# Kernel tuning notes

Measured on AMD Instinct MI355X. Metric: run time of the kernel, lower is better.

## Reference

```python
import jax, jax.numpy as jnp
import numpy as np

NUM_RBF = 300
RADIUS_RES = 0.1
GAMMA = 10.0
HIDDEN = 64
MB, ATOM = 32, 64


def setup_inputs() -> dict:
    key = jax.random.key(0)
    ks = jax.random.split(key, 12)
    def lin(kw, kb, fan_in, fan_out):
        lim = 1.0 / np.sqrt(fan_in)
        W = jax.random.uniform(kw, (fan_out, fan_in), jnp.float32, -lim, lim)
        b = jax.random.uniform(kb, (fan_out,), jnp.float32, -lim, lim)
        return W, b
    W1, b1 = lin(ks[0], ks[1], HIDDEN, HIDDEN)
    W2, b2 = lin(ks[2], ks[3], HIDDEN, HIDDEN)
    W3, b3 = lin(ks[4], ks[5], HIDDEN, HIDDEN)
    Wd1, bd1 = lin(ks[6], ks[7], NUM_RBF, HIDDEN)
    Wd2, bd2 = lin(ks[8], ks[9], HIDDEN, HIDDEN)
    x = jax.random.normal(ks[10], (MB, ATOM, HIDDEN), jnp.float32)
    dist = jax.random.uniform(ks[11], (MB, ATOM, ATOM), jnp.float32, 0.0, 10.0)
    return {"x": x, "dist": dist,
            "W1": W1, "b1": b1, "W2": W2, "b2": b2, "W3": W3, "b3": b3,
            "Wd1": Wd1, "bd1": bd1, "Wd2": Wd2, "bd2": bd2}


def reference(x, dist, W1, b1, W2, b2, W3, b3, Wd1, bd1, Wd2, bd2):
    sp = jax.nn.softplus
    # linear1 applied per-atom
    v = jnp.einsum('mic,oc->mio', x, W1) + b1                      # [mb, atom, h]
    # CFConv: gaussian RBF expansion of pairwise distances
    centers = jnp.arange(NUM_RBF, dtype=jnp.float32) * RADIUS_RES  # [rbf]
    rbf = jnp.exp(-GAMMA * (dist[..., None] - centers) ** 2)       # [mb, a, a, rbf]
    # 2-layer filter MLP on each pair
    f = sp(jnp.einsum('mijr,hr->mijh', rbf, Wd1) + bd1)            # [mb, a, a, h]
    f = sp(jnp.einsum('mijh,oh->mijo', f, Wd2) + bd2)              # [mb, a, a, h]
    # broadcast-multiply v over pairs and reduce over source atom i (dim=1)
    v = jnp.einsum('mic,mijc->mjc', v, f)                          # [mb, atom, h]
    v = sp(jnp.einsum('mic,oc->mio', v, W2) + b2)
    v = jnp.einsum('mic,oc->mio', v, W3) + b3
    return x + v
```

## Files before the change

kernel.cpp:

```cpp
#include <hip/hip_runtime.h>
#include <math.h>

#define MB_    32
#define ATOM_  64
#define HID_   64
#define NRBF_  300
#define GAMMA_ 10.0f
#define RES_   0.1f

#define TPTS      2001
#define TSTEP     0.005f
#define INV_TSTEP 200.0f

#define RWIN 28

#define T_OFF   0
#define T_SZ    (TPTS * 64)
#define V1_OFF  (T_OFF + T_SZ)
#define V1_SZ   (MB_ * 64 * 64)
#define W2T_OFF (V1_OFF + V1_SZ)
#define W3T_OFF (W2T_OFF + 4096)

__device__ __forceinline__ float sp_f(float x) {
    return fmaxf(x, 0.f) + log1pf(__expf(-fabsf(x)));
}

__global__ __launch_bounds__(256)
void schnet_prep(const float* __restrict__ x,   const float* __restrict__ W1,
                 const float* __restrict__ b1,  const float* __restrict__ W2,
                 const float* __restrict__ W3,  const float* __restrict__ Wd1,
                 const float* __restrict__ bd1, const float* __restrict__ Wd2,
                 const float* __restrict__ bd2, float* __restrict__ ws)
{
    __shared__ float smem[8320];
    const int tid = threadIdx.x;
    const int b   = blockIdx.x;

    if (b < MB_) {
        float* sx = smem;
        float* sw = smem + 4160;
        const float* xm = x + b * 4096;
        for (int e = tid; e < 4096; e += 256) {
            int i = e >> 6, c = e & 63;
            sx[i * 65 + c] = xm[e];
            sw[i * 65 + c] = W1[e];
        }
        __syncthreads();
        const int tx = tid & 15;
        const int ty = tid >> 4;
        float acc[4][4];
        #pragma unroll
        for (int aa = 0; aa < 4; ++aa)
            #pragma unroll
            for (int bb = 0; bb < 4; ++bb)
                acc[aa][bb] = b1[4 * tx + bb];
        #pragma unroll 8
        for (int k = 0; k < 64; ++k) {
            float xa[4], wb[4];
            #pragma unroll
            for (int aa = 0; aa < 4; ++aa) xa[aa] = sx[(4 * ty + aa) * 65 + k];
            #pragma unroll
            for (int bb = 0; bb < 4; ++bb) wb[bb] = sw[(4 * tx + bb) * 65 + k];
            #pragma unroll
            for (int aa = 0; aa < 4; ++aa)
                #pragma unroll
                for (int bb = 0; bb < 4; ++bb)
                    acc[aa][bb] = fmaf(xa[aa], wb[bb], acc[aa][bb]);
        }
        #pragma unroll
        for (int aa = 0; aa < 4; ++aa) {
            float4 v = make_float4(acc[aa][0], acc[aa][1], acc[aa][2], acc[aa][3]);
            *(float4*)(ws + V1_OFF + (b * 64 + 4 * ty + aa) * 64 + 4 * tx) = v;
        }
    } else if (b < MB_ + 501) {
        float* su = smem;
        const int sub = tid >> 6, c = tid & 63;
        const int s  = (b - MB_) * 4 + sub;
        const int se = min(s, TPTS - 1);
        const float d = se * TSTEP;

        int r0 = (int)ceilf((d - 1.35f) * 10.0f);
        r0 = max(r0, 0);

        float a0 = bd1[c], a1 = 0.f;
        const float* wrow1 = Wd1 + c * NRBF_ + r0;
        #pragma unroll
        for (int k = 0; k < RWIN; k += 2) {
            float t0 = fmaf(-RES_, (float)(r0 + k),     d);
            float t1 = fmaf(-RES_, (float)(r0 + k + 1), d);
            float w0 = __expf(-GAMMA_ * t0 * t0);
            float w1 = __expf(-GAMMA_ * t1 * t1);
            a0 = fmaf(w0, wrow1[k],     a0);
            a1 = fmaf(w1, wrow1[k + 1], a1);
        }
        su[sub * 64 + c] = sp_f(a0 + a1);
        __syncthreads();

        const float4* wrow2 = (const float4*)(Wd2 + c * 64);
        const float*  uu    = su + sub * 64;
        float s0 = bd2[c], s1 = 0.f, s2 = 0.f, s3 = 0.f;
        #pragma unroll
        for (int h4 = 0; h4 < 16; ++h4) {
            float4 wv = wrow2[h4];
            s0 = fmaf(wv.x, uu[4 * h4 + 0], s0);
            s1 = fmaf(wv.y, uu[4 * h4 + 1], s1);
            s2 = fmaf(wv.z, uu[4 * h4 + 2], s2);
            s3 = fmaf(wv.w, uu[4 * h4 + 3], s3);
        }
        if (s < TPTS)
            ws[T_OFF + s * 64 + c] = sp_f((s0 + s1) + (s2 + s3));
    } else {
        for (int e = tid; e < 4096; e += 256) {
            int o = e >> 6, c = e & 63;
            ws[W2T_OFF + c * 64 + o] = W2[e];
            ws[W3T_OFF + c * 64 + o] = W3[e];
        }
    }
}

__global__ __launch_bounds__(256)
void schnet_main(const float* __restrict__ x, const float* __restrict__ dist,
                 const float* __restrict__ b2, const float* __restrict__ b3,
                 const float* __restrict__ ws, float* __restrict__ out)
{
    __shared__ float sDist[64 * 4];
    __shared__ float sAgg [4 * 64];
    __shared__ float sV   [4 * 64];
    const int m   = blockIdx.x >> 4;
    const int j0  = (blockIdx.x & 15) * 4;
    const int tid = threadIdx.x;
    const int c   = tid & 63;
    const int p   = tid >> 6;

    if (tid < 64) {
        float4 dv = *(const float4*)(dist + (m * ATOM_ + tid) * ATOM_ + j0);
        *(float4*)(sDist + tid * 4) = dv;
    }
    __syncthreads();

    const float* Tb  = ws + T_OFF;
    const float* v1m = ws + V1_OFF + m * 4096;
    float acc = 0.f;
    #pragma unroll 8
    for (int ii = 0; ii < 64; ++ii) {
        float d  = sDist[ii * 4 + p];
        float f  = d * INV_TSTEP;
        int   s  = min((int)f, TPTS - 2);
        float fr = f - (float)s;
        const float* Tr = Tb + s * 64;
        float t0 = Tr[c], t1 = Tr[64 + c];
        float f2v = fmaf(fr, t1 - t0, t0);
        acc = fmaf(f2v, v1m[ii * 64 + c], acc);
    }
    sAgg[p * 64 + c] = acc;
    __syncthreads();

    {
        const float* W2t = ws + W2T_OFF;
        const float* ag  = sAgg + p * 64;
        float s0 = b2[c], s1 = 0.f;
        #pragma unroll 16
        for (int cc = 0; cc < 64; cc += 2) {
            s0 = fmaf(ag[cc],     W2t[cc * 64 + c],       s0);
            s1 = fmaf(ag[cc + 1], W2t[(cc + 1) * 64 + c], s1);
        }
        sV[p * 64 + c] = sp_f(s0 + s1);
    }
    __syncthreads();

    {
        const float* W3t = ws + W3T_OFF;
        const float* vv  = sV + p * 64;
        float s0 = b3[c], s1 = 0.f;
        #pragma unroll 16
        for (int oo = 0; oo < 64; oo += 2) {
            s0 = fmaf(vv[oo],     W3t[oo * 64 + c],       s0);
            s1 = fmaf(vv[oo + 1], W3t[(oo + 1) * 64 + c], s1);
        }
        const int idx = (m * ATOM_ + j0 + p) * HID_ + c;
        out[idx] = (s0 + s1) + x[idx];
    }
}

extern "C" void kernel_launch(void* const* d_in, const int* in_sizes, int n_in,
                              void* d_out, int out_size, void* d_ws, size_t ws_size,
                              hipStream_t stream) {
    const float* x   = (const float*)d_in[0];
    const float* dist= (const float*)d_in[1];
    const float* W1  = (const float*)d_in[2];
    const float* b1  = (const float*)d_in[3];
    const float* W2  = (const float*)d_in[4];
    const float* b2  = (const float*)d_in[5];
    const float* W3  = (const float*)d_in[6];
    const float* b3  = (const float*)d_in[7];
    const float* Wd1 = (const float*)d_in[8];
    const float* bd1 = (const float*)d_in[9];
    const float* Wd2 = (const float*)d_in[10];
    const float* bd2 = (const float*)d_in[11];
    float* out = (float*)d_out;
    float* ws  = (float*)d_ws;
    (void)in_sizes; (void)n_in; (void)out_size; (void)ws_size;

    schnet_prep<<<dim3(MB_ + 501 + 1), dim3(256), 0, stream>>>(
        x, W1, b1, W2, W3, Wd1, bd1, Wd2, bd2, ws);
    schnet_main<<<dim3(MB_ * 16), dim3(256), 0, stream>>>(
        x, dist, b2, b3, ws, out);
}
```

Measured before the change: 94.31 us.

## Fuse prep and main kernels into one cooperative kernel with grid sync

Merges the table-build/linear1 prep kernel and the main aggregation kernel into a single cooperative launch of 512 blocks separated by a grid-wide barrier. Each block now computes a slice of the filter table, a slice of linear1, and part of the W2/W3 transposes before the barrier. The aim is to remove the second kernel launch and its inter-kernel gap. In exchange it adds grid-sync cost, loads W1 redundantly into every block, and requires all 512 blocks to be co-resident.

```diff
diff --git a/kernel.cpp b/kernel.cpp
--- a/kernel.cpp
+++ b/kernel.cpp
@@ -1,5 +1,8 @@
 #include <hip/hip_runtime.h>
+#include <hip/hip_cooperative_groups.h>
 #include <math.h>
+
+namespace cg = cooperative_groups;
 
 #define MB_    32
 #define ATOM_  64
@@ -25,57 +28,52 @@
     return fmaxf(x, 0.f) + log1pf(__expf(-fabsf(x)));
 }
 
-__global__ __launch_bounds__(256)
-void schnet_prep(const float* __restrict__ x,   const float* __restrict__ W1,
-                 const float* __restrict__ b1,  const float* __restrict__ W2,
-                 const float* __restrict__ W3,  const float* __restrict__ Wd1,
-                 const float* __restrict__ bd1, const float* __restrict__ Wd2,
-                 const float* __restrict__ bd2, float* __restrict__ ws)
+__global__ __launch_bounds__(256, 2)
+void schnet_one(const float* __restrict__ x,   const float* __restrict__ dist,
+                const float* __restrict__ W1,  const float* __restrict__ b1,
+                const float* __restrict__ W2,  const float* __restrict__ b2,
+                const float* __restrict__ W3,  const float* __restrict__ b3,
+                const float* __restrict__ Wd1, const float* __restrict__ bd1,
+                const float* __restrict__ Wd2, const float* __restrict__ bd2,
+                float* __restrict__ ws,        float* __restrict__ out)
 {
-    __shared__ float smem[8320];
+    __shared__ float sw1 [64 * 65];
+    __shared__ float sxr [4 * 64];
+    __shared__ float su  [4 * 64];
+    __shared__ float sDist[64 * 4];
+    __shared__ float sAgg [4 * 64];
+    __shared__ float sV   [4 * 64];
+
+    const int b   = blockIdx.x;
     const int tid = threadIdx.x;
-    const int b   = blockIdx.x;
+    const int c   = tid & 63;
+    const int p   = tid >> 6;
 
-    if (b < MB_) {
-        float* sx = smem;
-        float* sw = smem + 4160;
-        const float* xm = x + b * 4096;
-        for (int e = tid; e < 4096; e += 256) {
-            int i = e >> 6, c = e & 63;
-            sx[i * 65 + c] = xm[e];
-            sw[i * 65 + c] = W1[e];
+    const int m  = b >> 4;
+    const int q  = b & 15;
+
+    for (int e = tid; e < 4096; e += 256) {
+        int o = e >> 6, cc = e & 63;
+        sw1[o * 65 + cc] = W1[e];
+    }
+    {
+        int row = tid >> 6, col = tid & 63;
+        sxr[row * 64 + col] = x[m * 4096 + (4 * q + row) * 64 + col];
+    }
+    __syncthreads();
+
+    {
+        float a0 = b1[c], a1 = 0.f;
+        #pragma unroll
+        for (int k = 0; k < 64; k += 2) {
+            a0 = fmaf(sxr[p * 64 + k],     sw1[c * 65 + k],     a0);
+            a1 = fmaf(sxr[p * 64 + k + 1], sw1[c * 65 + k + 1], a1);
         }
-        __syncthreads();
-        const int tx = tid & 15;
-        const int ty = tid >> 4;
-        float acc[4][4];
-        #pragma unroll
-        for (int aa = 0; aa < 4; ++aa)
-            #pragma unroll
-            for (int bb = 0; bb < 4; ++bb)
-                acc[aa][bb] = b1[4 * tx + bb];
-        #pragma unroll 8
-        for (int k = 0; k < 64; ++k) {
-            float xa[4], wb[4];
-            #pragma unroll
-            for (int aa = 0; aa < 4; ++aa) xa[aa] = sx[(4 * ty + aa) * 65 + k];
-            #pragma unroll
-            for (int bb = 0; bb < 4; ++bb) wb[bb] = sw[(4 * tx + bb) * 65 + k];
-            #pragma unroll
-            for (int aa = 0; aa < 4; ++aa)
-                #pragma unroll
-                for (int bb = 0; bb < 4; ++bb)
-                    acc[aa][bb] = fmaf(xa[aa], wb[bb], acc[aa][bb]);
-        }
-        #pragma unroll
-        for (int aa = 0; aa < 4; ++aa) {
-            float4 v = make_float4(acc[aa][0], acc[aa][1], acc[aa][2], acc[aa][3]);
-            *(float4*)(ws + V1_OFF + (b * 64 + 4 * ty + aa) * 64 + 4 * tx) = v;
-        }
-    } else if (b < MB_ + 501) {
-        float* su = smem;
-        const int sub = tid >> 6, c = tid & 63;
-        const int s  = (b - MB_) * 4 + sub;
+        ws[V1_OFF + (m * 64 + 4 * q + p) * 64 + c] = a0 + a1;
+    }
+
+    {
+        const int s  = 4 * b + p;
         const int se = min(s, TPTS - 1);
         const float d = se * TSTEP;
 
@@ -93,11 +91,11 @@
             a0 = fmaf(w0, wrow1[k],     a0);
             a1 = fmaf(w1, wrow1[k + 1], a1);
         }
-        su[sub * 64 + c] = sp_f(a0 + a1);
+        su[p * 64 + c] = sp_f(a0 + a1);
         __syncthreads();
 
         const float4* wrow2 = (const float4*)(Wd2 + c * 64);
-        const float*  uu    = su + sub * 64;
+        const float*  uu    = su + p * 64;
         float s0 = bd2[c], s1 = 0.f, s2 = 0.f, s3 = 0.f;
         #pragma unroll
         for (int h4 = 0; h4 < 16; ++h4) {
@@ -109,28 +107,19 @@
         }
         if (s < TPTS)
             ws[T_OFF + s * 64 + c] = sp_f((s0 + s1) + (s2 + s3));
-    } else {
-        for (int e = tid; e < 4096; e += 256) {
-            int o = e >> 6, c = e & 63;
-            ws[W2T_OFF + c * 64 + o] = W2[e];
-            ws[W3T_OFF + c * 64 + o] = W3[e];
-        }
     }
-}
 
-__global__ __launch_bounds__(256)
-void schnet_main(const float* __restrict__ x, const float* __restrict__ dist,
-                 const float* __restrict__ b2, const float* __restrict__ b3,
-                 const float* __restrict__ ws, float* __restrict__ out)
-{
-    __shared__ float sDist[64 * 4];
-    __shared__ float sAgg [4 * 64];
-    __shared__ float sV   [4 * 64];
-    const int m   = blockIdx.x >> 4;
-    const int j0  = (blockIdx.x & 15) * 4;
-    const int tid = threadIdx.x;
-    const int c   = tid & 63;
-    const int p   = tid >> 6;
+    if (b < 16) {
+        int e = b * 256 + tid;
+        int o = e >> 6, cc = e & 63;
+        ws[W2T_OFF + cc * 64 + o] = W2[e];
+        ws[W3T_OFF + cc * 64 + o] = W3[e];
+    }
+
+    __threadfence();
+    cg::this_grid().sync();
+
+    const int j0 = q * 4;
 
     if (tid < 64) {
         float4 dv = *(const float4*)(dist + (m * ATOM_ + tid) * ATOM_ + j0);
@@ -201,8 +190,10 @@
     float* ws  = (float*)d_ws;
     (void)in_sizes; (void)n_in; (void)out_size; (void)ws_size;
 
-    schnet_prep<<<dim3(MB_ + 501 + 1), dim3(256), 0, stream>>>(
-        x, W1, b1, W2, W3, Wd1, bd1, Wd2, bd2, ws);
-    schnet_main<<<dim3(MB_ * 16), dim3(256), 0, stream>>>(
-        x, dist, b2, b3, ws, out);
+    void* args[] = { (void*)&x, (void*)&dist, (void*)&W1, (void*)&b1,
+                     (void*)&W2, (void*)&b2,  (void*)&W3, (void*)&b3,
+                     (void*)&Wd1,(void*)&bd1, (void*)&Wd2,(void*)&bd2,
+                     (void*)&ws, (void*)&out };
+    hipLaunchCooperativeKernel((const void*)schnet_one, dim3(512), dim3(256),
+                               args, 0, stream);
 }
```

Result: slower. 217.5 us (+130.7%).
